# Optimization experiments

Hardware: AMD Instinct MI355X
Metric: run time of the kernel (lower is better)

Reference implementation:

```python
import math
import jax, jax.numpy as jnp
import numpy as np

N_HEAD = 32
LAYER_NUMBER = 10  # cancels out: beta*alibi*L + alpha*QK^T*L = alibi + QK^T/sqrt(d)


def build_alibi(seq_len, n_head, dtype):
    # Faithful port of BLOOM's build_alibi_tensor -> [n_head, 1, seq_len]
    cp2 = 2 ** math.floor(math.log2(n_head))
    base = 2.0 ** (-(2.0 ** -(math.log2(cp2) - 3)))
    slopes = base ** np.arange(1, 1 + cp2)
    if cp2 != n_head:
        extra_base = 2.0 ** (-(2.0 ** -(math.log2(2 * cp2) - 3)))
        num_rem = min(cp2, n_head - cp2)
        slopes = np.concatenate([slopes, extra_base ** np.arange(1, 1 + 2 * num_rem, 2)])
    alibi = slopes[:, None, None] * np.arange(seq_len)[None, None, :]
    return jnp.asarray(alibi, dtype)


def setup_inputs() -> dict:
    key = jax.random.key(0)
    ks = jax.random.split(key, 6)
    B, S, H = 4, 1024, 4096
    return {
        "hidden_states": jax.random.normal(ks[0], (B, S, H), jnp.float32),
        "residual": jax.random.normal(ks[1], (B, S, H), jnp.float32),
        "qkv_w": jax.random.normal(ks[2], (3 * H, H), jnp.float32) * 0.02,
        "qkv_b": jnp.zeros((3 * H,), jnp.float32),
        "dense_w": jax.random.normal(ks[3], (H, H), jnp.float32) * 0.02,
        "dense_b": jnp.zeros((H,), jnp.float32),
    }


def reference(hidden_states, residual, qkv_w, qkv_b, dense_w, dense_b):
    B, S, H = hidden_states.shape
    nh = N_HEAD
    d = H // nh
    # fused qkv projection: [B,S,3H] -> [B,S,nh,3d] -> split
    mixed = (hidden_states @ qkv_w.T + qkv_b).reshape(B, S, nh, 3 * d)
    q, k, v = jnp.split(mixed, 3, axis=-1)  # each [B,S,nh,d]

    alibi = build_alibi(S, nh, hidden_states.dtype)  # [nh,1,S]
    # beta*alibi + alpha*QK^T, then *layer_number in scaled softmax == alibi + QK^T/sqrt(d)
    scores = jnp.einsum("bqhd,bkhd->bhqk", q, k) / math.sqrt(d) + alibi[None]  # [B,nh,S,S]

    causal = jnp.tril(jnp.ones((S, S), bool))  # [S,S], True = attend
    scores = jnp.where(causal, scores, jnp.asarray(-10000.0, scores.dtype))
    # softmax in fp32 (attention_softmax_in_fp32), then zero masked entries like *(~padded_causal_mask)
    probs = jax.nn.softmax(scores.astype(jnp.float32), axis=-1) * causal
    probs = probs.astype(v.dtype)

    ctx = jnp.einsum("bhqk,bkhd->bqhd", probs, v).reshape(B, S, H)
    out = ctx @ dense_w.T + dense_b + residual  # dropout_add with p=0 / eval
    return out
```

## Files before the change

### kernel.cpp

```cpp
#include <hip/hip_runtime.h>
#include <hip/hip_bf16.h>

typedef __attribute__((ext_vector_type(8))) short bf16x8;
typedef __attribute__((ext_vector_type(4))) short short4v;
typedef __attribute__((ext_vector_type(4))) float f32x4;

#define MFMA16(A, B, C) __builtin_amdgcn_mfma_f32_16x16x32_bf16((A), (B), (C), 0, 0, 0)
#define GLDS16(g, l)                                                            \
  __builtin_amdgcn_global_load_lds(                                             \
      (const __attribute__((address_space(1))) void*)(g),                       \
      (__attribute__((address_space(3))) void*)(l), 16, 0, 0)

__device__ __forceinline__ short f2bf(float f) {
  union { float f; unsigned u; } v; v.f = f;
  return (short)((v.u + 0x7fffu + ((v.u >> 16) & 1u)) >> 16);
}

__device__ __forceinline__ void blk_barrier() {
  asm volatile("" ::: "memory");
  __builtin_amdgcn_s_barrier();
  asm volatile("" ::: "memory");
}

__global__ __launch_bounds__(256) void cvt3_kernel(const float* __restrict__ in0,
                                                   short* __restrict__ out0, int n0,
                                                   const float* __restrict__ in1,
                                                   short* __restrict__ out1, int n1,
                                                   const float* __restrict__ in2,
                                                   short* __restrict__ out2, int n2) {
  int i = blockIdx.x * 256 + threadIdx.x;
  const int stride = gridDim.x * 256;
  const int total = n0 + n1 + n2;
  for (; i < total; i += stride) {
    const float* src;
    short* dst;
    int j = i;
    if (j < n0) { src = in0; dst = out0; }
    else if ((j -= n0) < n1) { src = in1; dst = out1; }
    else { j -= n1; src = in2; dst = out2; }
    f32x4 v = ((const f32x4*)src)[j];
    short4v o;
    o[0] = f2bf(v[0]); o[1] = f2bf(v[1]); o[2] = f2bf(v[2]); o[3] = f2bf(v[3]);
    ((short4v*)dst)[j] = o;
  }
}

__global__ __launch_bounds__(512, 2) void gemm_bt8(const short* __restrict__ A,
                                                   const short* __restrict__ B,
                                                   const float* __restrict__ bias,
                                                   const float* __restrict__ resid,
                                                   short* __restrict__ Cb,
                                                   float* __restrict__ Cf,
                                                   int Mtiles, int Nn, int K, int mode) {
  __shared__ short sA[2][2][8192];
  __shared__ short sB[2][2][8192];
  const int tid = threadIdx.x;
  const int w = tid >> 6, l = tid & 63;
  const int wm = w >> 2, wn = w & 3;
  const int fr = l & 15, g4 = l >> 4, sx = l & 7;

  const int nwg = gridDim.x;
  const int qq = nwg >> 3, rr = nwg & 7;
  const int xcd = blockIdx.x & 7, sub = blockIdx.x >> 3;
  const int swz = (xcd < rr ? xcd * (qq + 1) : rr * (qq + 1) + (xcd - rr) * qq) + sub;
  const int rowBase = (swz % Mtiles) * 256;
  const int colBase = (swz / Mtiles) * 256;

  const int NT = K >> 6;
  const int swcol = ((l & 7) ^ (l >> 3)) * 8;
  const short* Ag = A + (size_t)(rowBase + w * 8 + (l >> 3)) * K + swcol;
  const short* Bg = B + (size_t)(colBase + w * 8 + (l >> 3)) * K + swcol;
  const size_t q1 = (size_t)64 * K;
  const size_t hh = (size_t)128 * K;

#define STAGE_A(buf, h, ko)                                     \
  GLDS16(Ag + (h) * hh + (ko), &sA[buf][h][w * 512]);           \
  GLDS16(Ag + (h) * hh + q1 + (ko), &sA[buf][h][(8 + w) * 512]);
#define STAGE_B(buf, h, ko)                                     \
  GLDS16(Bg + (h) * hh + (ko), &sB[buf][h][w * 512]);           \
  GLDS16(Bg + (h) * hh + q1 + (ko), &sB[buf][h][(8 + w) * 512]);
#define RD_A(buf, m, ks) \
  (*(const bf16x8*)&sA[buf][wm][(((m) * 16 + fr) << 6) + ((((ks) * 4 + g4) ^ sx) << 3)])
#define RD_B(buf, nf, ks) \
  (*(const bf16x8*)&sB[buf][wn >> 1][((((wn & 1) * 64) + (nf) * 16 + fr) << 6) + ((((ks) * 4 + g4) ^ sx) << 3)])

  f32x4 acc[8][4];
#pragma unroll
  for (int m = 0; m < 8; m++)
#pragma unroll
    for (int n = 0; n < 4; n++) acc[m][n] = (f32x4)(0.0f);

  STAGE_A(0, 0, 0); STAGE_A(0, 1, 0);
  STAGE_B(0, 0, 0); STAGE_B(0, 1, 0);

  for (int t = 0; t < NT; ++t) {
    const int cur = t & 1, nxt = cur ^ 1;
    const size_t ko = (size_t)(t + 1) << 6;
    bf16x8 bfr[4][2], af[2][2];
    if (t + 1 < NT) {
      STAGE_A(nxt, 0, ko); STAGE_A(nxt, 1, ko);
      asm volatile("s_waitcnt vmcnt(4)" ::: "memory");
    } else {
      asm volatile("s_waitcnt vmcnt(0)" ::: "memory");
    }
    blk_barrier();
#pragma unroll
    for (int nf = 0; nf < 4; nf++) {
      bfr[nf][0] = RD_B(cur, nf, 0);
      bfr[nf][1] = RD_B(cur, nf, 1);
    }
    af[0][0] = RD_A(cur, 0, 0); af[0][1] = RD_A(cur, 0, 1);
    af[1][0] = RD_A(cur, 1, 0); af[1][1] = RD_A(cur, 1, 1);
    __builtin_amdgcn_s_setprio(1);
#pragma unroll
    for (int mi = 0; mi < 2; mi++)
#pragma unroll
      for (int nf = 0; nf < 4; nf++) {
        acc[mi][nf] = MFMA16(af[mi][0], bfr[nf][0], acc[mi][nf]);
        acc[mi][nf] = MFMA16(af[mi][1], bfr[nf][1], acc[mi][nf]);
      }
    __builtin_amdgcn_s_setprio(0);
    blk_barrier();
#pragma unroll
    for (int p = 1; p < 4; p++) {
      af[0][0] = RD_A(cur, 2 * p, 0);     af[0][1] = RD_A(cur, 2 * p, 1);
      af[1][0] = RD_A(cur, 2 * p + 1, 0); af[1][1] = RD_A(cur, 2 * p + 1, 1);
      if (p == 1 && t + 1 < NT) {
        STAGE_B(nxt, 0, ko); STAGE_B(nxt, 1, ko);
      }
      blk_barrier();
      __builtin_amdgcn_s_setprio(1);
#pragma unroll
      for (int mi = 0; mi < 2; mi++)
#pragma unroll
        for (int nf = 0; nf < 4; nf++) {
          acc[2 * p + mi][nf] = MFMA16(af[mi][0], bfr[nf][0], acc[2 * p + mi][nf]);
          acc[2 * p + mi][nf] = MFMA16(af[mi][1], bfr[nf][1], acc[2 * p + mi][nf]);
        }
      __builtin_amdgcn_s_setprio(0);
      blk_barrier();
    }
  }

#pragma unroll
  for (int m = 0; m < 8; m++) {
    const int row0 = rowBase + wm * 128 + m * 16 + g4 * 4;
#pragma unroll
    for (int n = 0; n < 4; n++) {
      const int col = colBase + wn * 64 + n * 16 + fr;
      const float bc = bias[col];
#pragma unroll
      for (int j = 0; j < 4; j++) {
        const size_t idx = (size_t)(row0 + j) * Nn + col;
        const float v = acc[m][n][j] + bc;
        if (mode == 0) Cb[idx] = f2bf(v);
        else Cf[idx] = v + resid[idx];
      }
    }
  }
#undef STAGE_A
#undef STAGE_B
#undef RD_A
#undef RD_B
}

__global__ __launch_bounds__(512, 4) void gemm_bt(const short* __restrict__ A,
                                                  const short* __restrict__ B,
                                                  const float* __restrict__ bias,
                                                  const float* __restrict__ resid,
                                                  short* __restrict__ Cb,
                                                  float* __restrict__ Cf,
                                                  int Mtiles, int Nn, int K, int mode) {
  __shared__ short sA[2][128 * 32];
  __shared__ short sB[2][256 * 32];
  const int tid = threadIdx.x;
  const int w = tid >> 6, l = tid & 63;
  const int wm = w >> 2, wn = w & 3;
  const int fr = l & 15, g4 = l >> 4;
  const int slotx = (g4 ^ ((fr >> 1) & 3)) << 3;

  const int nwg = gridDim.x;
  const int qq = nwg >> 3, rr = nwg & 7;
  const int xcd = blockIdx.x & 7, sub = blockIdx.x >> 3;
  const int swz = (xcd < rr ? xcd * (qq + 1) : rr * (qq + 1) + (xcd - rr) * qq) + sub;
  const int rowBase = (swz % Mtiles) * 128;
  const int colBase = (swz / Mtiles) * 256;

  const int NT = K >> 5;
  const int scol = ((l & 3) ^ ((l >> 3) & 3)) << 3;
  const short* Ag = A + (size_t)(rowBase + w * 16 + (l >> 2)) * K + scol;
  const short* Bg0 = B + (size_t)(colBase + w * 16 + (l >> 2)) * K + scol;
  const short* Bg1 = Bg0 + (size_t)128 * K;

  f32x4 acc[4][4];
#pragma unroll
  for (int m = 0; m < 4; m++)
#pragma unroll
    for (int n = 0; n < 4; n++) acc[m][n] = (f32x4)(0.0f);

  GLDS16(Ag, &sA[0][w * 512]);
  GLDS16(Bg0, &sB[0][w * 512]);
  GLDS16(Bg1, &sB[0][(8 + w) * 512]);

  for (int t = 0; t < NT; ++t) {
    const int cur = t & 1, nxt = cur ^ 1;
    const int ko = (t + 1) << 5;
    if (t + 1 < NT) {
      GLDS16(Ag + ko, &sA[nxt][w * 512]);
      GLDS16(Bg0 + ko, &sB[nxt][w * 512]);
      GLDS16(Bg1 + ko, &sB[nxt][(8 + w) * 512]);
      asm volatile("s_waitcnt vmcnt(3)" ::: "memory");
    } else {
      asm volatile("s_waitcnt vmcnt(0)" ::: "memory");
    }
    blk_barrier();

    bf16x8 af[4], bfr[4];
#pragma unroll
    for (int m = 0; m < 4; m++)
      af[m] = *(const bf16x8*)&sA[cur][(wm * 64 + m * 16 + fr) * 32 + slotx];
#pragma unroll
    for (int nf = 0; nf < 4; nf++)
      bfr[nf] = *(const bf16x8*)&sB[cur][(wn * 64 + nf * 16 + fr) * 32 + slotx];
    __builtin_amdgcn_s_setprio(1);
#pragma unroll
    for (int m = 0; m < 4; m++)
#pragma unroll
      for (int nf = 0; nf < 4; nf++)
        acc[m][nf] = MFMA16(af[m], bfr[nf], acc[m][nf]);
    __builtin_amdgcn_s_setprio(0);
    blk_barrier();
  }

#pragma unroll
  for (int m = 0; m < 4; m++) {
    const int row0 = rowBase + wm * 64 + m * 16 + g4 * 4;
#pragma unroll
    for (int n = 0; n < 4; n++) {
      const int col = colBase + wn * 64 + n * 16 + fr;
      const float bc = bias[col];
#pragma unroll
      for (int j = 0; j < 4; j++) {
        const size_t idx = (size_t)(row0 + j) * Nn + col;
        const float v = acc[m][n][j] + bc;
        if (mode == 0) Cb[idx] = f2bf(v);
        else Cf[idx] = v + resid[idx];
      }
    }
  }
}

__global__ __launch_bounds__(256) void vtrans_kernel(const short* __restrict__ mixed,
                                                     short* __restrict__ vt) {
  __shared__ short tl[64][132];
  const int tid = threadIdx.x;
  const int st = blockIdx.x;
  const int bh = blockIdx.y;
  const int b = bh >> 5, h = bh & 31;
  const short* src = mixed + (size_t)(b * 1024 + st * 64) * 12288 + h * 384 + 256;
#pragma unroll
  for (int it = 0; it < 8; it++) {
    int idx = (tid + it * 256) * 4;
    int row = idx >> 7, col = idx & 127;
    *(short4v*)&tl[row][col] = *(const short4v*)(src + row * 12288 + col);
  }
  __syncthreads();
  short* dst = vt + (size_t)bh * 128 * 1024 + st * 64;
#pragma unroll
  for (int it = 0; it < 8; it++) {
    int o = (tid + it * 256) * 4;
    int d = o >> 6, t4 = o & 63;
    short4v w;
    w[0] = tl[t4][d]; w[1] = tl[t4 + 1][d]; w[2] = tl[t4 + 2][d]; w[3] = tl[t4 + 3][d];
    *(short4v*)(dst + d * 1024 + t4) = w;
  }
}

__global__ __launch_bounds__(256, 2) void attn_kernel(const short* __restrict__ mixed,
                                                      const short* __restrict__ vt,
                                                      short* __restrict__ ctx) {
  __shared__ short sK[2][64 * 128];
  __shared__ short sV[2][128 * 64];
  __shared__ unsigned p_lds[4][16 * 36];
  const int tid = threadIdx.x;
  const int w = tid >> 6, l = tid & 63;
  const int g = l >> 4, f = l & 15, f7 = l & 7;

  const int bidx = blockIdx.x;
  const int xcd = bidx & 7, idx = bidx >> 3;
  const int bh = (xcd << 4) | (idx >> 4);
  const int qt = idx & 15;
  const int b = bh >> 5, h = bh & 31;
  const int qw = qt * 64 + w * 16;
  const float scale = 0.08838834764831845f;
  const float slope = exp2f(-0.25f * (float)(h + 1));

  const short* qptr = mixed + (size_t)b * 1024 * 12288 + h * 384;
  const short* kptr = qptr + 128;
  const short* vtp = vt + (size_t)bh * 128 * 1024;

  bf16x8 qf[4];
  {
    const short* qrow = qptr + (size_t)(qw + f) * 12288 + (g << 3);
#pragma unroll
    for (int ks = 0; ks < 4; ks++) qf[ks] = *(const bf16x8*)(qrow + ks * 32);
  }

#define STAGE_K(buf, kt)                                                        \
  {                                                                             \
    _Pragma("unroll") for (int c4 = 0; c4 < 4; c4++) {                          \
      const int c = c4 * 4 + w;                                                 \
      const int r = c * 4 + (l >> 4);                                           \
      GLDS16(kptr + (size_t)((kt) + r) * 12288 + (((l & 15) ^ (r & 7)) << 3),   \
             &sK[buf][c << 9]);                                                 \
    }                                                                           \
  }
#define STAGE_V(buf, kt)                                                        \
  {                                                                             \
    _Pragma("unroll") for (int c4 = 0; c4 < 4; c4++) {                          \
      const int c = c4 * 4 + w;                                                 \
      const int r = c * 8 + (l >> 3);                                           \
      GLDS16(vtp + (size_t)r * 1024 + (kt) + (((l & 7) ^ (r & 7)) << 3),        \
             &sV[buf][c << 9]);                                                 \
    }                                                                           \
  }

  f32x4 acc[8];
#pragma unroll
  for (int n = 0; n < 8; n++) acc[n] = (f32x4)(0.0f);
  float mrun = -1e30f, lrun = 0.0f;
  const int q = qw + f;
  unsigned* pw = p_lds[w];

  const int TT = qt + 1;
  STAGE_K(0, 0);
  STAGE_V(0, 0);

  for (int t = 0; t < TT; ++t) {
    const int cur = t & 1, nxt = cur ^ 1;
    const int kt = t << 6;
    if (t + 1 < TT) {
      STAGE_K(nxt, kt + 64);
      STAGE_V(nxt, kt + 64);
      asm volatile("s_waitcnt vmcnt(8)" ::: "memory");
    } else {
      asm volatile("s_waitcnt vmcnt(0)" ::: "memory");
    }
    blk_barrier();

    f32x4 s[4];
#pragma unroll
    for (int ksub = 0; ksub < 4; ksub++) {
      s[ksub] = (f32x4)(0.0f);
      const int r = ksub * 16 + f;
#pragma unroll
      for (int ks = 0; ks < 4; ks++) {
        bf16x8 kf = *(const bf16x8*)&sK[cur][(r << 7) + ((((ks << 2) + g) ^ f7) << 3)];
        s[ksub] = MFMA16(kf, qf[ks], s[ksub]);
      }
    }

    float ev[4][4];
    float tmax = -1e30f;
#pragma unroll
    for (int ksub = 0; ksub < 4; ksub++)
#pragma unroll
      for (int j = 0; j < 4; j++) {
        const int k = kt + ksub * 16 + g * 4 + j;
        float v = s[ksub][j] * scale + slope * (float)k;
        if (k > q) v = -1e30f;
        ev[ksub][j] = v;
        tmax = fmaxf(tmax, v);
      }
    tmax = fmaxf(tmax, __shfl_xor(tmax, 16));
    tmax = fmaxf(tmax, __shfl_xor(tmax, 32));
    const float mnew = fmaxf(mrun, tmax);
    const float asc = __expf(mrun - mnew);
    float psum = 0.0f;
    unsigned* pr = pw + f * 36;
#pragma unroll
    for (int ksub = 0; ksub < 4; ksub++) {
      float e0 = __expf(ev[ksub][0] - mnew);
      float e1 = __expf(ev[ksub][1] - mnew);
      float e2 = __expf(ev[ksub][2] - mnew);
      float e3 = __expf(ev[ksub][3] - mnew);
      psum += (e0 + e1) + (e2 + e3);
      unsigned w0 = (unsigned)(unsigned short)f2bf(e0) |
                    ((unsigned)(unsigned short)f2bf(e1) << 16);
      unsigned w1 = (unsigned)(unsigned short)f2bf(e2) |
                    ((unsigned)(unsigned short)f2bf(e3) << 16);
      pr[ksub * 8 + g * 2] = w0;
      pr[ksub * 8 + g * 2 + 1] = w1;
    }
    psum += __shfl_xor(psum, 16);
    psum += __shfl_xor(psum, 32);
    lrun = lrun * asc + psum;
    mrun = mnew;

    float ascB[4];
#pragma unroll
    for (int j = 0; j < 4; j++) ascB[j] = __shfl(asc, 20 * g + j);
#pragma unroll
    for (int n = 0; n < 8; n++)
#pragma unroll
      for (int j = 0; j < 4; j++) acc[n][j] *= ascB[j];

    bf16x8 pa0 = *(const bf16x8*)(pw + f * 36 + (g << 2));
    bf16x8 pa1 = *(const bf16x8*)(pw + f * 36 + 16 + (g << 2));
#pragma unroll
    for (int n = 0; n < 8; n++) {
      const int dr = (n << 4) + f;
      bf16x8 vf0 = *(const bf16x8*)&sV[cur][(dr << 6) + ((g ^ f7) << 3)];
      acc[n] = MFMA16(pa0, vf0, acc[n]);
      bf16x8 vf1 = *(const bf16x8*)&sV[cur][(dr << 6) + (((4 + g) ^ f7) << 3)];
      acc[n] = MFMA16(pa1, vf1, acc[n]);
    }
    blk_barrier();
  }

  const float linv = 1.0f / lrun;
  float invB[4];
#pragma unroll
  for (int j = 0; j < 4; j++) invB[j] = __shfl(linv, 20 * g + j);
  const int trow = b * 1024 + qw + (g << 2);
#pragma unroll
  for (int n = 0; n < 8; n++) {
    const int col = h * 128 + (n << 4) + f;
#pragma unroll
    for (int j = 0; j < 4; j++)
      ctx[(size_t)(trow + j) * 4096 + col] = f2bf(acc[n][j] * invB[j]);
  }
#undef STAGE_K
#undef STAGE_V
}

extern "C" void kernel_launch(void* const* d_in, const int* in_sizes, int n_in,
                              void* d_out, int out_size, void* d_ws, size_t ws_size,
                              hipStream_t stream) {
  const float* hs = (const float*)d_in[0];
  const float* resid = (const float*)d_in[1];
  const float* qkv_w = (const float*)d_in[2];
  const float* qkv_b = (const float*)d_in[3];
  const float* dense_w = (const float*)d_in[4];
  const float* dense_b = (const float*)d_in[5];
  float* out = (float*)d_out;

  short* hs_b = (short*)d_ws;
  short* wqkv_b = hs_b + (size_t)16777216;
  short* wd_b = wqkv_b + (size_t)50331648;
  short* mixed = wd_b + (size_t)16777216;
  short* vt = wqkv_b;
  short* ctx = hs_b;

  cvt3_kernel<<<2048, 256, 0, stream>>>(hs, hs_b, 16777216 / 4,
                                        qkv_w, wqkv_b, 50331648 / 4,
                                        dense_w, wd_b, 16777216 / 4);
  gemm_bt8<<<dim3(48 * 16), 512, 0, stream>>>(hs_b, wqkv_b, qkv_b, nullptr,
                                              mixed, nullptr, 16, 12288, 4096, 0);
  vtrans_kernel<<<dim3(16, 128), 256, 0, stream>>>(mixed, vt);
  attn_kernel<<<2048, 256, 0, stream>>>(mixed, vt, ctx);
  gemm_bt<<<dim3(32 * 16), 512, 0, stream>>>(ctx, wd_b, dense_b, resid,
                                             nullptr, out, 32, 4096, 4096, 1);
}
```

Baseline: 795.3 us.

## Fuse V transpose into QKV GEMM epilogue and drop vtrans kernel

The QKV GEMM epilogue now writes the V slice of each head straight into a transposed layout, stored in place inside the mixed buffer's V region with each head's 128 columns reinterpreted as [d][t]. The attention kernel's V staging reads from that layout, and the separate transpose kernel plus its launch are removed. This avoids a full extra read and write pass over V. In exchange, V stores in the epilogue become 4-element scattered writes with a different access pattern, and V staging loads in attention use a strided 12288-element row pitch.

Result: no change. 784.1 us, median of 4 (-1.4%).

```diff
diff --git a/kernel.cpp b/kernel.cpp
--- a/kernel.cpp
+++ b/kernel.cpp
@@ -149,12 +149,27 @@
     for (int n = 0; n < 4; n++) {
       const int col = colBase + wn * 64 + n * 16 + fr;
       const float bc = bias[col];
-#pragma unroll
-      for (int j = 0; j < 4; j++) {
-        const size_t idx = (size_t)(row0 + j) * Nn + col;
-        const float v = acc[m][n][j] + bc;
-        if (mode == 0) Cb[idx] = f2bf(v);
-        else Cf[idx] = v + resid[idx];
+      if (mode == 0) {
+        const int cmod = col % 384;
+        if (cmod >= 256) {
+          const int h = col / 384, d = cmod - 256;
+          const int b = row0 >> 10, t0 = row0 & 1023;
+          short4v pv;
+#pragma unroll
+          for (int j = 0; j < 4; j++) pv[j] = f2bf(acc[m][n][j] + bc);
+          *(short4v*)&Cb[(size_t)(b * 1024 + d * 8 + (t0 >> 7)) * Nn +
+                         h * 384 + 256 + (t0 & 127)] = pv;
+        } else {
+#pragma unroll
+          for (int j = 0; j < 4; j++)
+            Cb[(size_t)(row0 + j) * Nn + col] = f2bf(acc[m][n][j] + bc);
+        }
+      } else {
+#pragma unroll
+        for (int j = 0; j < 4; j++) {
+          const size_t idx = (size_t)(row0 + j) * Nn + col;
+          Cf[idx] = acc[m][n][j] + bc + resid[idx];
+        }
       }
     }
   }
@@ -250,34 +265,7 @@
   }
 }
 
-__global__ __launch_bounds__(256) void vtrans_kernel(const short* __restrict__ mixed,
-                                                     short* __restrict__ vt) {
-  __shared__ short tl[64][132];
-  const int tid = threadIdx.x;
-  const int st = blockIdx.x;
-  const int bh = blockIdx.y;
-  const int b = bh >> 5, h = bh & 31;
-  const short* src = mixed + (size_t)(b * 1024 + st * 64) * 12288 + h * 384 + 256;
-#pragma unroll
-  for (int it = 0; it < 8; it++) {
-    int idx = (tid + it * 256) * 4;
-    int row = idx >> 7, col = idx & 127;
-    *(short4v*)&tl[row][col] = *(const short4v*)(src + row * 12288 + col);
-  }
-  __syncthreads();
-  short* dst = vt + (size_t)bh * 128 * 1024 + st * 64;
-#pragma unroll
-  for (int it = 0; it < 8; it++) {
-    int o = (tid + it * 256) * 4;
-    int d = o >> 6, t4 = o & 63;
-    short4v w;
-    w[0] = tl[t4][d]; w[1] = tl[t4 + 1][d]; w[2] = tl[t4 + 2][d]; w[3] = tl[t4 + 3][d];
-    *(short4v*)(dst + d * 1024 + t4) = w;
-  }
-}
-
 __global__ __launch_bounds__(256, 2) void attn_kernel(const short* __restrict__ mixed,
-                                                      const short* __restrict__ vt,
                                                       short* __restrict__ ctx) {
   __shared__ short sK[2][64 * 128];
   __shared__ short sV[2][128 * 64];
@@ -297,7 +285,7 @@
 
   const short* qptr = mixed + (size_t)b * 1024 * 12288 + h * 384;
   const short* kptr = qptr + 128;
-  const short* vtp = vt + (size_t)bh * 128 * 1024;
+  const short* vbase = qptr + 256;
 
   bf16x8 qf[4];
   {
@@ -320,7 +308,8 @@
     _Pragma("unroll") for (int c4 = 0; c4 < 4; c4++) {                          \
       const int c = c4 * 4 + w;                                                 \
       const int r = c * 8 + (l >> 3);                                           \
-      GLDS16(vtp + (size_t)r * 1024 + (kt) + (((l & 7) ^ (r & 7)) << 3),        \
+      const int ts = ((l & 7) ^ (r & 7)) << 3;                                  \
+      GLDS16(vbase + (size_t)(r * 8 + ((kt) >> 7)) * 12288 + (((kt) & 127) + ts), \
              &sV[buf][c << 9]);                                                 \
     }                                                                           \
   }
@@ -449,7 +438,6 @@
   short* wqkv_b = hs_b + (size_t)16777216;
   short* wd_b = wqkv_b + (size_t)50331648;
   short* mixed = wd_b + (size_t)16777216;
-  short* vt = wqkv_b;
   short* ctx = hs_b;
 
   cvt3_kernel<<<2048, 256, 0, stream>>>(hs, hs_b, 16777216 / 4,
@@ -457,8 +445,7 @@
                                         dense_w, wd_b, 16777216 / 4);
   gemm_bt8<<<dim3(48 * 16), 512, 0, stream>>>(hs_b, wqkv_b, qkv_b, nullptr,
                                               mixed, nullptr, 16, 12288, 4096, 0);
-  vtrans_kernel<<<dim3(16, 128), 256, 0, stream>>>(mixed, vt);
-  attn_kernel<<<2048, 256, 0, stream>>>(mixed, vt, ctx);
+  attn_kernel<<<2048, 256, 0, stream>>>(mixed, ctx);
   gemm_bt<<<dim3(32 * 16), 512, 0, stream>>>(ctx, wd_b, dense_b, resid,
                                              nullptr, out, 32, 4096, 4096, 1);
 }
```
